# Performance work log

Hardware: AMD Instinct MI355X
Metric: run time of the kernel (lower is better)

The kernel has to match this reference:

```python
import jax, jax.numpy as jnp
import numpy as np

EPS = 1e-12  # F.normalize eps


def sage_conv(x, src, dst, n_nodes, W_l, b_l, W_r):
    """PyG SAGEConv with mean aggregation and L2 normalize.
    out = lin_l(mean_{j in N(i)} x_j) + lin_r(x_i), then row-wise L2 normalize.
    """
    # mean-aggregate neighbor features: scatter-add then divide by in-degree
    msg_sum = jax.ops.segment_sum(x[src], dst, num_segments=n_nodes)  # [N, F]
    deg = jax.ops.segment_sum(jnp.ones_like(dst, dtype=x.dtype), dst,
                              num_segments=n_nodes)                   # [N]
    agg = msg_sum / jnp.maximum(deg, 1.0)[:, None]
    out = agg @ W_l + b_l + x @ W_r                                   # [N, out]
    norm = jnp.sqrt(jnp.sum(out * out, axis=-1, keepdims=True))
    return out / jnp.maximum(norm, EPS)


def setup_inputs() -> dict:
    key = jax.random.key(0)
    ks = jax.random.split(key, 8)
    N, E, D_IN, D_H, D_OUT = 100000, 320000, 256, 64, 4
    x = jax.random.normal(ks[0], (N, D_IN), dtype=jnp.float32)
    edge_index = jax.random.randint(ks[1], (2, E), 0, N, dtype=jnp.int32)
    s1 = 1.0 / np.sqrt(D_IN)
    s2 = 1.0 / np.sqrt(D_H)
    W1_l = jax.random.uniform(ks[2], (D_IN, D_H), jnp.float32, -s1, s1)
    b1_l = jnp.zeros((D_H,), jnp.float32)
    W1_r = jax.random.uniform(ks[3], (D_IN, D_H), jnp.float32, -s1, s1)
    W2_l = jax.random.uniform(ks[4], (D_H, D_OUT), jnp.float32, -s2, s2)
    b2_l = jnp.zeros((D_OUT,), jnp.float32)
    W2_r = jax.random.uniform(ks[5], (D_H, D_OUT), jnp.float32, -s2, s2)
    return {"x": x, "edge_index": edge_index,
            "W1_l": W1_l, "b1_l": b1_l, "W1_r": W1_r,
            "W2_l": W2_l, "b2_l": b2_l, "W2_r": W2_r}


def reference(x, edge_index, W1_l, b1_l, W1_r, W2_l, b2_l, W2_r):
    # eval mode: dropout is identity
    n_nodes = x.shape[0]
    src, dst = edge_index[0], edge_index[1]
    h = jax.nn.relu(sage_conv(x, src, dst, n_nodes, W1_l, b1_l, W1_r))
    out = sage_conv(h, src, dst, n_nodes, W2_l, b2_l, W2_r)
    return out
```

## Files before the change

kernel.cpp:

```cpp
#include <hip/hip_runtime.h>

#define DIN 256
#define DH  64
#define DOUT 4
#define CAP 32

typedef __attribute__((ext_vector_type(8))) short bf16x8;
typedef __attribute__((ext_vector_type(4))) float f32x4;

__device__ __forceinline__ short f2bf(float f) {
    unsigned int u = __float_as_uint(f);
    unsigned int r = (u + 0x7FFFu + ((u >> 16) & 1u)) >> 16;
    return (short)r;
}
__device__ __forceinline__ short f2bf_trunc(float f) {
    return (short)(__float_as_uint(f) >> 16);
}
__device__ __forceinline__ float bf2f(short h) {
    return __uint_as_float(((unsigned int)(unsigned short)h) << 16);
}

__global__ void fillprep_kernel(const int* __restrict__ src, const int* __restrict__ dst,
                                int* __restrict__ cnt, int* __restrict__ bucket,
                                const float* __restrict__ Wl, const float* __restrict__ Wr,
                                short* __restrict__ WTh, short* __restrict__ WTl,
                                int E, int FB)
{
    if ((int)blockIdx.x >= FB) {
        const int n = blockIdx.x - FB;
        const int k = threadIdx.x;
        const float v = (n < 64) ? Wl[k * 64 + n] : Wr[k * 64 + (n - 64)];
        const short hi = f2bf(v);
        const short lo = f2bf(v - bf2f(hi));
        WTh[n * 256 + k] = hi;
        WTl[n * 256 + k] = lo;
        return;
    }
    const int e = blockIdx.x * 256 + threadIdx.x;
    if (e >= E) return;
    const int d = dst[e];
    const int p = atomicAdd(&cnt[d], 1);
    if (p < CAP) bucket[(size_t)d * CAP + p] = src[e];
}

#define XS_LD 40
__global__ __launch_bounds__(256, 4) void gemm1_mfma(
    const float* __restrict__ x, const short* __restrict__ WTh,
    const short* __restrict__ WTl, float* __restrict__ y, int N)
{
    __shared__ short xsh[2][64 * XS_LD];
    __shared__ short xsl[2][64 * XS_LD];

    const int tid  = threadIdx.x;
    const int wave = tid >> 6;
    const int lane = tid & 63;
    const int lm   = lane & 15;
    const int quad = lane >> 4;
    const int brow = blockIdx.x * 64;

    const int xr    = tid >> 2;
    const int xk    = (tid & 3) * 8;
    const int row_g = brow + xr;
    const bool xvalid = (row_g < N);
    const float* xptr = x + (size_t)row_g * DIN + xk;
    const int xs_off = xr * XS_LD + xk;

    const int col0 = wave * 32 + lm;
    const size_t wb0 = (size_t)col0 * 256 + quad * 8;
    const size_t wb1 = (size_t)(col0 + 16) * 256 + quad * 8;

    f32x4 acc[4][2];
    #pragma unroll
    for (int mt = 0; mt < 4; ++mt)
        #pragma unroll
        for (int nt = 0; nt < 2; ++nt)
            acc[mt][nt] = (f32x4){0.f, 0.f, 0.f, 0.f};

    {
        float4 a, b;
        if (xvalid) {
            a = ((const float4*)xptr)[0];
            b = ((const float4*)xptr)[1];
        } else {
            a = b = make_float4(0.f, 0.f, 0.f, 0.f);
        }
        bf16x8 ph, pl;
        float fv[8] = {a.x, a.y, a.z, a.w, b.x, b.y, b.z, b.w};
        #pragma unroll
        for (int j = 0; j < 8; ++j) {
            const short hi = f2bf_trunc(fv[j]);
            ph[j] = hi;
            pl[j] = f2bf_trunc(fv[j] - bf2f(hi));
        }
        *(bf16x8*)(&xsh[0][xs_off]) = ph;
        *(bf16x8*)(&xsl[0][xs_off]) = pl;
    }
    bf16x8 wh_cur[2], wl_cur[2];
    wh_cur[0] = *(const bf16x8*)(WTh + wb0);
    wh_cur[1] = *(const bf16x8*)(WTh + wb1);
    wl_cur[0] = *(const bf16x8*)(WTl + wb0);
    wl_cur[1] = *(const bf16x8*)(WTl + wb1);
    __syncthreads();

    #pragma unroll
    for (int k = 0; k < 8; ++k) {
        const int buf = k & 1;

        float4 na, nb;
        bf16x8 wh_nxt[2], wl_nxt[2];
        if (k < 7) {
            const int kc = (k + 1) * 32;
            if (xvalid) {
                na = ((const float4*)(xptr + kc))[0];
                nb = ((const float4*)(xptr + kc))[1];
            } else {
                na = nb = make_float4(0.f, 0.f, 0.f, 0.f);
            }
            wh_nxt[0] = *(const bf16x8*)(WTh + wb0 + kc);
            wh_nxt[1] = *(const bf16x8*)(WTh + wb1 + kc);
            wl_nxt[0] = *(const bf16x8*)(WTl + wb0 + kc);
            wl_nxt[1] = *(const bf16x8*)(WTl + wb1 + kc);
        }

        #pragma unroll
        for (int mt = 0; mt < 4; ++mt) {
            const int aoff = (mt * 16 + lm) * XS_LD + quad * 8;
            const bf16x8 ah = *(const bf16x8*)(&xsh[buf][aoff]);
            const bf16x8 al = *(const bf16x8*)(&xsl[buf][aoff]);
            #pragma unroll
            for (int nt = 0; nt < 2; ++nt) {
                acc[mt][nt] = __builtin_amdgcn_mfma_f32_16x16x32_bf16(
                    ah, wh_cur[nt], acc[mt][nt], 0, 0, 0);
                acc[mt][nt] = __builtin_amdgcn_mfma_f32_16x16x32_bf16(
                    ah, wl_cur[nt], acc[mt][nt], 0, 0, 0);
                acc[mt][nt] = __builtin_amdgcn_mfma_f32_16x16x32_bf16(
                    al, wh_cur[nt], acc[mt][nt], 0, 0, 0);
            }
        }

        if (k < 7) {
            bf16x8 ph, pl;
            float fv[8] = {na.x, na.y, na.z, na.w, nb.x, nb.y, nb.z, nb.w};
            #pragma unroll
            for (int j = 0; j < 8; ++j) {
                const short hi = f2bf_trunc(fv[j]);
                ph[j] = hi;
                pl[j] = f2bf_trunc(fv[j] - bf2f(hi));
            }
            *(bf16x8*)(&xsh[buf ^ 1][xs_off]) = ph;
            *(bf16x8*)(&xsl[buf ^ 1][xs_off]) = pl;
            #pragma unroll
            for (int nt = 0; nt < 2; ++nt) {
                wh_cur[nt] = wh_nxt[nt];
                wl_cur[nt] = wl_nxt[nt];
            }
            __syncthreads();
        }
    }

    #pragma unroll
    for (int mt = 0; mt < 4; ++mt) {
        #pragma unroll
        for (int r = 0; r < 4; ++r) {
            const int rg = brow + mt * 16 + quad * 4 + r;
            if (rg < N) {
                const int col = wave * 32 + lm;
                float* yp = y + (size_t)rg * 128 + col;
                yp[0]  = acc[mt][0][r];
                yp[16] = acc[mt][1][r];
            }
        }
    }
}

__device__ __forceinline__ float gemm2_butterfly(float hv, float4 wl, float4 wr, int lane) {
    float p0 = hv * wl.x, p1 = hv * wl.y, p2 = hv * wl.z, p3 = hv * wl.w;
    float p4 = hv * wr.x, p5 = hv * wr.y, p6 = hv * wr.z, p7 = hv * wr.w;
    const bool b0 = (lane & 1) != 0;
    float s0_ = b0 ? p0 : p4;
    float s1_ = b0 ? p1 : p5;
    float s2_ = b0 ? p2 : p6;
    float s3_ = b0 ? p3 : p7;
    float q0 = (b0 ? p4 : p0) + __shfl_xor(s0_, 1, 64);
    float q1 = (b0 ? p5 : p1) + __shfl_xor(s1_, 1, 64);
    float q2 = (b0 ? p6 : p2) + __shfl_xor(s2_, 1, 64);
    float q3 = (b0 ? p7 : p3) + __shfl_xor(s3_, 1, 64);
    const bool b1b = (lane & 2) != 0;
    float t0 = b1b ? q0 : q2;
    float t1 = b1b ? q1 : q3;
    float r0 = (b1b ? q2 : q0) + __shfl_xor(t0, 2, 64);
    float r1 = (b1b ? q3 : q1) + __shfl_xor(t1, 2, 64);
    const bool b2 = (lane & 4) != 0;
    float u0 = b2 ? r0 : r1;
    float zv = (b2 ? r1 : r0) + __shfl_xor(u0, 4, 64);
    zv += __shfl_xor(zv, 8, 64);
    zv += __shfl_xor(zv, 16, 64);
    zv += __shfl_xor(zv, 32, 64);
    return zv;
}

__global__ __launch_bounds__(256) void fused1_kernel(
    const float* __restrict__ y, const int* __restrict__ cnt, const int* __restrict__ bucket,
    const float* __restrict__ b1, const float* __restrict__ W2l, const float* __restrict__ W2r,
    float* __restrict__ z, int N)
{
    const int wave = threadIdx.x >> 6;
    const int lane = threadIdx.x & 63;
    const int half = lane >> 5;
    const int l5   = lane & 31;
    const int base = (blockIdx.x * 4 + wave) * 2;
    if (base >= N) return;
    const int iA = base;
    const bool hasB = (base + 1 < N);
    const int iB = hasB ? base + 1 : base;

    const int degA = cnt[iA];
    const int degB = cnt[iB];
    const int ddA = (degA < CAP) ? degA : CAP;
    const int ddB = (degB < CAP) ? degB : CAP;

    const int myn = bucket[(size_t)(half ? iB : iA) * CAP + l5];

    float accA = 0.f, accB = 0.f;
    const int jm = (ddA > ddB) ? ddA : ddB;
    for (int j = 0; j < jm; j += 2) {
        const int sA0 = __shfl(myn, j, 64);
        const int sA1 = __shfl(myn, j + 1, 64);
        const int sB0 = __shfl(myn, 32 + j, 64);
        const int sB1 = __shfl(myn, 33 + j, 64);
        const int cA0 = (j     < ddA) ? sA0 : 0;
        const int cA1 = (j + 1 < ddA) ? sA1 : 0;
        const int cB0 = (j     < ddB) ? sB0 : 0;
        const int cB1 = (j + 1 < ddB) ? sB1 : 0;
        const float vA0 = y[(size_t)cA0 * 128 + lane];
        const float vA1 = y[(size_t)cA1 * 128 + lane];
        const float vB0 = y[(size_t)cB0 * 128 + lane];
        const float vB1 = y[(size_t)cB1 * 128 + lane];
        if (j + 1 < ddA)  accA += vA0 + vA1;
        else if (j < ddA) accA += vA0;
        if (j + 1 < ddB)  accB += vB0 + vB1;
        else if (j < ddB) accB += vB0;
    }

    const float dinvA = 1.0f / fmaxf((float)degA, 1.0f);
    const float dinvB = 1.0f / fmaxf((float)degB, 1.0f);
    const float bl = b1[lane];
    float vA = accA * dinvA + bl + y[(size_t)iA * 128 + 64 + lane];
    float vB = accB * dinvB + bl + y[(size_t)iB * 128 + 64 + lane];

    float ssA = vA * vA, ssB = vB * vB;
    #pragma unroll
    for (int m = 32; m >= 1; m >>= 1) {
        ssA += __shfl_xor(ssA, m, 64);
        ssB += __shfl_xor(ssB, m, 64);
    }
    const float invA = 1.0f / fmaxf(sqrtf(ssA), 1e-12f);
    const float invB = 1.0f / fmaxf(sqrtf(ssB), 1e-12f);
    const float hvA = fmaxf(vA * invA, 0.f);
    const float hvB = fmaxf(vB * invB, 0.f);

    const float4 wl = *(const float4*)(W2l + lane * 4);
    const float4 wr = *(const float4*)(W2r + lane * 4);
    const float zvA = gemm2_butterfly(hvA, wl, wr, lane);
    const float zvB = gemm2_butterfly(hvB, wl, wr, lane);

    const int ch = 4 * (lane & 1) + (lane & 2) + ((lane >> 2) & 1);
    if (lane < 8) {
        z[(size_t)iA * 8 + ch] = zvA;
        if (hasB) z[(size_t)iB * 8 + ch] = zvB;
    }
}

__global__ void fused2_kernel(const float* __restrict__ z, const int* __restrict__ cnt,
                              const int* __restrict__ bucket, const float* __restrict__ b2,
                              float* __restrict__ out, int N)
{
    const int i = blockIdx.x * blockDim.x + threadIdx.x;
    if (i >= N) return;
    const int deg = cnt[i];
    const int dd = (deg < CAP) ? deg : CAP;

    float4 t[8];
    #pragma unroll
    for (int j = 0; j < 8; ++j) {
        int s = bucket[(size_t)i * CAP + ((j < dd) ? j : 0)];
        s = (j < dd) ? s : i;
        t[j] = *(const float4*)(z + (size_t)s * 8);
    }

    float4 acc = make_float4(0.f, 0.f, 0.f, 0.f);
    #pragma unroll
    for (int j = 0; j < 8; ++j) {
        if (j < dd) {
            acc.x += t[j].x; acc.y += t[j].y; acc.z += t[j].z; acc.w += t[j].w;
        }
    }
    for (int j = 8; j < dd; ++j) {
        const int s = bucket[(size_t)i * CAP + j];
        const float4 u = *(const float4*)(z + (size_t)s * 8);
        acc.x += u.x; acc.y += u.y; acc.z += u.z; acc.w += u.w;
    }

    const float dinv = 1.0f / fmaxf((float)deg, 1.0f);
    const float4 r  = *(const float4*)(z + (size_t)i * 8 + 4);
    const float4 bb = *(const float4*)(b2);
    float4 o;
    o.x = acc.x * dinv + bb.x + r.x;
    o.y = acc.y * dinv + bb.y + r.y;
    o.z = acc.z * dinv + bb.z + r.z;
    o.w = acc.w * dinv + bb.w + r.w;
    const float ss = o.x * o.x + o.y * o.y + o.z * o.z + o.w * o.w;
    const float inv = 1.0f / fmaxf(sqrtf(ss), 1e-12f);
    o.x *= inv; o.y *= inv; o.z *= inv; o.w *= inv;
    *(float4*)(out + (size_t)i * 4) = o;
}

extern "C" void kernel_launch(void* const* d_in, const int* in_sizes, int n_in,
                              void* d_out, int out_size, void* d_ws, size_t ws_size,
                              hipStream_t stream)
{
    const float* x    = (const float*)d_in[0];
    const int*   ei   = (const int*)d_in[1];
    const float* W1l  = (const float*)d_in[2];
    const float* b1l  = (const float*)d_in[3];
    const float* W1r  = (const float*)d_in[4];
    const float* W2l  = (const float*)d_in[5];
    const float* b2l  = (const float*)d_in[6];
    const float* W2r  = (const float*)d_in[7];
    float* out = (float*)d_out;

    const int N = in_sizes[0] / DIN;
    const int E = in_sizes[1] / 2;
    const int* src = ei;
    const int* dst = ei + E;

    char* ws = (char*)d_ws;
    size_t woff = 0;
    auto alloc = [&](size_t bytes) {
        void* p = ws + woff;
        woff += (bytes + 255) & ~(size_t)255;
        return p;
    };
    float* y      = (float*)alloc((size_t)N * 128 * 4);
    float* z      = (float*)alloc((size_t)N * 8 * 4);
    short* WTh    = (short*)alloc((size_t)128 * 256 * 2);
    short* WTl    = (short*)alloc((size_t)128 * 256 * 2);
    int*   cnt    = (int*)alloc((size_t)N * 4);
    int*   bucket = (int*)alloc((size_t)N * CAP * 4);

    hipMemsetAsync(cnt, 0, (size_t)N * 4, stream);

    const int FB = (E + 255) / 256;
    fillprep_kernel<<<FB + 128, 256, 0, stream>>>(src, dst, cnt, bucket,
                                                  W1l, W1r, WTh, WTl, E, FB);

    gemm1_mfma<<<(N + 63) / 64, 256, 0, stream>>>(x, WTh, WTl, y, N);

    fused1_kernel<<<(N + 7) / 8, 256, 0, stream>>>(y, cnt, bucket, b1l, W2l, W2r, z, N);

    fused2_kernel<<<(N + 255) / 256, 256, 0, stream>>>(z, cnt, bucket, b2l, out, N);
}
```

Measured before the change: 255.2 us.

## Load whole x tile into LDS via direct global_load_lds, split bf16 at read

```diff
diff --git a/kernel.cpp b/kernel.cpp
--- a/kernel.cpp
+++ b/kernel.cpp
@@ -43,79 +43,58 @@
     if (p < CAP) bucket[(size_t)d * CAP + p] = src[e];
 }
 
-#define XS_LD 40
+#define RX_LD 260
 __global__ __launch_bounds__(256, 4) void gemm1_mfma(
     const float* __restrict__ x, const short* __restrict__ WTh,
     const short* __restrict__ WTl, float* __restrict__ y, int N)
 {
-    __shared__ short xsh[2][64 * XS_LD];
-    __shared__ short xsl[2][64 * XS_LD];
+    __shared__ float rawx[32 * RX_LD];
 
     const int tid  = threadIdx.x;
     const int wave = tid >> 6;
     const int lane = tid & 63;
     const int lm   = lane & 15;
     const int quad = lane >> 4;
-    const int brow = blockIdx.x * 64;
-
-    const int xr    = tid >> 2;
-    const int xk    = (tid & 3) * 8;
-    const int row_g = brow + xr;
-    const bool xvalid = (row_g < N);
-    const float* xptr = x + (size_t)row_g * DIN + xk;
-    const int xs_off = xr * XS_LD + xk;
+    const int brow = blockIdx.x * 32;
+
+    {
+        const int srow = wave * 8;
+        #pragma unroll
+        for (int j = 0; j < 8; ++j) {
+            const int rowg = min(brow + srow + j, N - 1);
+            __builtin_amdgcn_global_load_lds(
+                (const __attribute__((address_space(1))) unsigned int*)
+                    (x + (size_t)rowg * DIN + lane * 4),
+                (__attribute__((address_space(3))) unsigned int*)
+                    &rawx[(srow + j) * RX_LD],
+                16, 0, 0);
+        }
+    }
 
     const int col0 = wave * 32 + lm;
     const size_t wb0 = (size_t)col0 * 256 + quad * 8;
     const size_t wb1 = (size_t)(col0 + 16) * 256 + quad * 8;
 
-    f32x4 acc[4][2];
-    #pragma unroll
-    for (int mt = 0; mt < 4; ++mt)
+    f32x4 acc[2][2];
+    #pragma unroll
+    for (int mt = 0; mt < 2; ++mt)
         #pragma unroll
         for (int nt = 0; nt < 2; ++nt)
             acc[mt][nt] = (f32x4){0.f, 0.f, 0.f, 0.f};
 
-    {
-        float4 a, b;
-        if (xvalid) {
-            a = ((const float4*)xptr)[0];
-            b = ((const float4*)xptr)[1];
-        } else {
-            a = b = make_float4(0.f, 0.f, 0.f, 0.f);
-        }
-        bf16x8 ph, pl;
-        float fv[8] = {a.x, a.y, a.z, a.w, b.x, b.y, b.z, b.w};
-        #pragma unroll
-        for (int j = 0; j < 8; ++j) {
-            const short hi = f2bf_trunc(fv[j]);
-            ph[j] = hi;
-            pl[j] = f2bf_trunc(fv[j] - bf2f(hi));
-        }
-        *(bf16x8*)(&xsh[0][xs_off]) = ph;
-        *(bf16x8*)(&xsl[0][xs_off]) = pl;
-    }
     bf16x8 wh_cur[2], wl_cur[2];
     wh_cur[0] = *(const bf16x8*)(WTh + wb0);
     wh_cur[1] = *(const bf16x8*)(WTh + wb1);
     wl_cur[0] = *(const bf16x8*)(WTl + wb0);
     wl_cur[1] = *(const bf16x8*)(WTl + wb1);
+
     __syncthreads();
 
     #pragma unroll
     for (int k = 0; k < 8; ++k) {
-        const int buf = k & 1;
-
-        float4 na, nb;
         bf16x8 wh_nxt[2], wl_nxt[2];
         if (k < 7) {
             const int kc = (k + 1) * 32;
-            if (xvalid) {
-                na = ((const float4*)(xptr + kc))[0];
-                nb = ((const float4*)(xptr + kc))[1];
-            } else {
-                na = nb = make_float4(0.f, 0.f, 0.f, 0.f);
-            }
             wh_nxt[0] = *(const bf16x8*)(WTh + wb0 + kc);
             wh_nxt[1] = *(const bf16x8*)(WTh + wb1 + kc);
             wl_nxt[0] = *(const bf16x8*)(WTl + wb0 + kc);
@@ -123,10 +102,20 @@
         }
 
         #pragma unroll
-        for (int mt = 0; mt < 4; ++mt) {
-            const int aoff = (mt * 16 + lm) * XS_LD + quad * 8;
-            const bf16x8 ah = *(const bf16x8*)(&xsh[buf][aoff]);
-            const bf16x8 al = *(const bf16x8*)(&xsl[buf][aoff]);
+        for (int mt = 0; mt < 2; ++mt) {
+            const float* rp = &rawx[(mt * 16 + lm) * RX_LD + k * 32 + quad * 8];
+            const float4 r0 = ((const float4*)rp)[0];
+            const float4 r1 = ((const float4*)rp)[1];
+            bf16x8 ah, al;
+            {
+                float fv[8] = {r0.x, r0.y, r0.z, r0.w, r1.x, r1.y, r1.z, r1.w};
+                #pragma unroll
+                for (int j = 0; j < 8; ++j) {
+                    const short hi = f2bf_trunc(fv[j]);
+                    ah[j] = hi;
+                    al[j] = f2bf_trunc(fv[j] - bf2f(hi));
+                }
+            }
             #pragma unroll
             for (int nt = 0; nt < 2; ++nt) {
                 acc[mt][nt] = __builtin_amdgcn_mfma_f32_16x16x32_bf16(
@@ -139,27 +128,16 @@
         }
 
         if (k < 7) {
-            bf16x8 ph, pl;
-            float fv[8] = {na.x, na.y, na.z, na.w, nb.x, nb.y, nb.z, nb.w};
-            #pragma unroll
-            for (int j = 0; j < 8; ++j) {
-                const short hi = f2bf_trunc(fv[j]);
-                ph[j] = hi;
-                pl[j] = f2bf_trunc(fv[j] - bf2f(hi));
-            }
-            *(bf16x8*)(&xsh[buf ^ 1][xs_off]) = ph;
-            *(bf16x8*)(&xsl[buf ^ 1][xs_off]) = pl;
             #pragma unroll
             for (int nt = 0; nt < 2; ++nt) {
                 wh_cur[nt] = wh_nxt[nt];
                 wl_cur[nt] = wl_nxt[nt];
             }
-            __syncthreads();
-        }
-    }
-
-    #pragma unroll
-    for (int mt = 0; mt < 4; ++mt) {
+        }
+    }
+
+    #pragma unroll
+    for (int mt = 0; mt < 2; ++mt) {
         #pragma unroll
         for (int r = 0; r < 4; ++r) {
             const int rg = brow + mt * 16 + quad * 4 + r;
@@ -354,7 +332,7 @@
     fillprep_kernel<<<FB + 128, 256, 0, stream>>>(src, dst, cnt, bucket,
                                                   W1l, W1r, WTh, WTl, E, FB);
 
-    gemm1_mfma<<<(N + 63) / 64, 256, 0, stream>>>(x, WTh, WTl, y, N);
+    gemm1_mfma<<<(N + 31) / 32, 256, 0, stream>>>(x, WTh, WTl, y, N);
 
     fused1_kernel<<<(N + 7) / 8, 256, 0, stream>>>(y, cnt, bucket, b1l, W2l, W2r, z, N);
 
```

Measured after the change: 274.6 us. 7.6% more time.

## Merge edge bucketing into GEMM launch, fold count zeroing into weight prep, unroll gather

Applied to the files above, without the earlier changes.

```diff
diff --git a/kernel.cpp b/kernel.cpp
--- a/kernel.cpp
+++ b/kernel.cpp
@@ -20,14 +20,12 @@
     return __uint_as_float(((unsigned int)(unsigned short)h) << 16);
 }
 
-__global__ void fillprep_kernel(const int* __restrict__ src, const int* __restrict__ dst,
-                                int* __restrict__ cnt, int* __restrict__ bucket,
-                                const float* __restrict__ Wl, const float* __restrict__ Wr,
-                                short* __restrict__ WTh, short* __restrict__ WTl,
-                                int E, int FB)
-{
-    if ((int)blockIdx.x >= FB) {
-        const int n = blockIdx.x - FB;
+__global__ void wprep_zero_kernel(const float* __restrict__ Wl, const float* __restrict__ Wr,
+                                  short* __restrict__ WTh, short* __restrict__ WTl,
+                                  int* __restrict__ cnt, int N)
+{
+    if ((int)blockIdx.x < 128) {
+        const int n = blockIdx.x;
         const int k = threadIdx.x;
         const float v = (n < 64) ? Wl[k * 64 + n] : Wr[k * 64 + (n - 64)];
         const short hi = f2bf(v);
@@ -36,20 +34,33 @@
         WTl[n * 256 + k] = lo;
         return;
     }
-    const int e = blockIdx.x * 256 + threadIdx.x;
-    if (e >= E) return;
-    const int d = dst[e];
-    const int p = atomicAdd(&cnt[d], 1);
-    if (p < CAP) bucket[(size_t)d * CAP + p] = src[e];
+    const int t4 = (blockIdx.x - 128) * 256 + threadIdx.x;
+    const int n4 = N >> 2;
+    if (t4 < n4) ((int4*)cnt)[t4] = make_int4(0, 0, 0, 0);
+    if (t4 == 0)
+        for (int r = N & ~3; r < N; ++r) cnt[r] = 0;
 }
 
 #define XS_LD 40
-__global__ __launch_bounds__(256, 4) void gemm1_mfma(
+__global__ __launch_bounds__(256, 4) void gemm_scatter_kernel(
     const float* __restrict__ x, const short* __restrict__ WTh,
-    const short* __restrict__ WTl, float* __restrict__ y, int N)
+    const short* __restrict__ WTl, float* __restrict__ y,
+    const int* __restrict__ src, const int* __restrict__ dst,
+    int* __restrict__ cnt, int* __restrict__ bucket,
+    int N, int E, int NB)
 {
     __shared__ short xsh[2][64 * XS_LD];
     __shared__ short xsl[2][64 * XS_LD];
+
+    if ((int)blockIdx.x >= NB) {
+        const int e = ((int)blockIdx.x - NB) * 256 + threadIdx.x;
+        if (e < E) {
+            const int d = dst[e];
+            const int p = atomicAdd(&cnt[d], 1);
+            if (p < CAP) bucket[(size_t)d * CAP + p] = src[e];
+        }
+        return;
+    }
 
     const int tid  = threadIdx.x;
     const int wave = tid >> 6;
@@ -223,23 +234,39 @@
 
     float accA = 0.f, accB = 0.f;
     const int jm = (ddA > ddB) ? ddA : ddB;
-    for (int j = 0; j < jm; j += 2) {
-        const int sA0 = __shfl(myn, j, 64);
-        const int sA1 = __shfl(myn, j + 1, 64);
-        const int sB0 = __shfl(myn, 32 + j, 64);
-        const int sB1 = __shfl(myn, 33 + j, 64);
+    for (int j = 0; j < jm; j += 4) {
+        const int sA0 = __shfl(myn, j,      64);
+        const int sA1 = __shfl(myn, j + 1,  64);
+        const int sA2 = __shfl(myn, j + 2,  64);
+        const int sA3 = __shfl(myn, j + 3,  64);
+        const int sB0 = __shfl(myn, 32 + j,     64);
+        const int sB1 = __shfl(myn, 33 + j,     64);
+        const int sB2 = __shfl(myn, 34 + j,     64);
+        const int sB3 = __shfl(myn, 35 + j,     64);
         const int cA0 = (j     < ddA) ? sA0 : 0;
         const int cA1 = (j + 1 < ddA) ? sA1 : 0;
+        const int cA2 = (j + 2 < ddA) ? sA2 : 0;
+        const int cA3 = (j + 3 < ddA) ? sA3 : 0;
         const int cB0 = (j     < ddB) ? sB0 : 0;
         const int cB1 = (j + 1 < ddB) ? sB1 : 0;
+        const int cB2 = (j + 2 < ddB) ? sB2 : 0;
+        const int cB3 = (j + 3 < ddB) ? sB3 : 0;
         const float vA0 = y[(size_t)cA0 * 128 + lane];
         const float vA1 = y[(size_t)cA1 * 128 + lane];
+        const float vA2 = y[(size_t)cA2 * 128 + lane];
+        const float vA3 = y[(size_t)cA3 * 128 + lane];
         const float vB0 = y[(size_t)cB0 * 128 + lane];
         const float vB1 = y[(size_t)cB1 * 128 + lane];
-        if (j + 1 < ddA)  accA += vA0 + vA1;
-        else if (j < ddA) accA += vA0;
-        if (j + 1 < ddB)  accB += vB0 + vB1;
-        else if (j < ddB) accB += vB0;
+        const float vB2 = y[(size_t)cB2 * 128 + lane];
+        const float vB3 = y[(size_t)cB3 * 128 + lane];
+        if (j + 1 < ddA)      accA += vA0 + vA1;
+        else if (j < ddA)     accA += vA0;
+        if (j + 1 < ddB)      accB += vB0 + vB1;
+        else if (j < ddB)     accB += vB0;
+        if (j + 3 < ddA)      accA += vA2 + vA3;
+        else if (j + 2 < ddA) accA += vA2;
+        if (j + 3 < ddB)      accB += vB2 + vB3;
+        else if (j + 2 < ddB) accB += vB2;
     }
 
     const float dinvA = 1.0f / fmaxf((float)degA, 1.0f);
@@ -348,13 +375,13 @@
     int*   cnt    = (int*)alloc((size_t)N * 4);
     int*   bucket = (int*)alloc((size_t)N * CAP * 4);
 
-    hipMemsetAsync(cnt, 0, (size_t)N * 4, stream);
-
-    const int FB = (E + 255) / 256;
-    fillprep_kernel<<<FB + 128, 256, 0, stream>>>(src, dst, cnt, bucket,
-                                                  W1l, W1r, WTh, WTl, E, FB);
-
-    gemm1_mfma<<<(N + 63) / 64, 256, 0, stream>>>(x, WTh, WTl, y, N);
+    const int ZB = ((N >> 2) + 255) / 256;
+    wprep_zero_kernel<<<128 + ZB, 256, 0, stream>>>(W1l, W1r, WTh, WTl, cnt, N);
+
+    const int NB = (N + 63) / 64;
+    const int SB = (E + 255) / 256;
+    gemm_scatter_kernel<<<NB + SB, 256, 0, stream>>>(x, WTh, WTl, y,
+                                                     src, dst, cnt, bucket, N, E, NB);
 
     fused1_kernel<<<(N + 7) / 8, 256, 0, stream>>>(y, cnt, bucket, b1l, W2l, W2r, z, N);
 
```

After: 235.6 us. 1.08x faster.
